# Kernel optimization log

Measured on AMD Instinct MI355X. Metric: run time of the kernel, lower is better.

Reference implementation:

```python
import jax, jax.numpy as jnp
import numpy as np

N, D, H2, E = 4096, 1024, 4096, 8  # tokens, input_dim, 2*hidden_dim, num_experts
H = H2 // 2


def setup_inputs() -> dict:
    key = jax.random.key(0)
    k1, k2, k3 = jax.random.split(key, 3)
    x = jax.random.normal(k1, (N, D), dtype=jnp.float32)
    expert_weights = jax.random.normal(k2, (E, D, H2), dtype=jnp.float32) * (1.0 / np.sqrt(D))
    expert_indices = jax.random.randint(k3, (N,), 0, E, dtype=jnp.int32)
    return {"x": x, "expert_weights": expert_weights, "expert_indices": expert_indices}


def reference(x, expert_weights, expert_indices):
    # Grouped GEMM equivalent: each token n is processed by expert e = expert_indices[n]:
    #   h_n = x_n @ W_e            -> [2H]
    #   out_n = silu(h[:H]) * h[H:] (SwiGLU)
    # jit-friendly dense-dispatch: project with all experts, then gather the assigned one.
    h_all = jnp.einsum('nd,edh->neh', x, expert_weights)            # [N, E, 2H]
    h = jnp.take_along_axis(h_all, expert_indices[:, None, None].astype(jnp.int32), axis=1)[:, 0]  # [N, 2H]
    a, b = h[:, :H], h[:, H:]
    return jax.nn.silu(a) * b                                        # [N, H]
```

## Files before the change

kernel.cpp:

```cpp
#include <hip/hip_runtime.h>
#include <hip/hip_bf16.h>

#define N_TOK 4096
#define DIM   1024
#define H2V   4096
#define HV    2048
#define NE    8
#define BM    128
#define BN    64
#define BK    64
#define NTHR  256
#define KSTEPS (DIM / BK)
#define ROW_TILES (N_TOK / BM)

#define WS_COUNTS 0
#define WS_BASE   64
#define WS_SLOTS  128
#define WS_XPERM  66560

typedef __attribute__((ext_vector_type(4))) float  f32x4;
typedef __attribute__((ext_vector_type(8))) short  s16x8;

__device__ __forceinline__ unsigned short f2bf(float f) {
    union { __hip_bfloat16 h; unsigned short u; } v;
    v.h = __float2bfloat16(f);
    return v.u;
}

__global__ void k_init(int* __restrict__ counts) {
    if (threadIdx.x < NE) counts[threadIdx.x] = 0;
}

__global__ void k_scatter(const int* __restrict__ idx, int* __restrict__ counts,
                          unsigned short* __restrict__ slots) {
    int n = blockIdx.x * blockDim.x + threadIdx.x;
    if (n < N_TOK) {
        int e = idx[n];
        int p = atomicAdd(&counts[e], 1);
        slots[e * N_TOK + p] = (unsigned short)n;
    }
}

__global__ void k_base(const int* __restrict__ counts, int* __restrict__ base) {
    if (threadIdx.x == 0) {
        int b = 0;
#pragma unroll
        for (int e = 0; e < NE; ++e) { base[e] = b; b += counts[e]; }
        base[NE] = b;
    }
}

__global__ void k_gather(const float* __restrict__ X, const int* __restrict__ base,
                         const unsigned short* __restrict__ slots,
                         unsigned short* __restrict__ Xp) {
    const int r    = blockIdx.x * 4 + (threadIdx.x >> 6);
    const int lane = threadIdx.x & 63;
    int e = 0;
#pragma unroll
    for (int i = 0; i < NE - 1; ++i) if (r >= base[i + 1]) e = i + 1;
    const int tok = slots[e * N_TOK + (r - base[e])];
    const float* src = X + (size_t)tok * DIM + lane * 16;
    unsigned short* dst = Xp + (size_t)r * DIM + lane * 16;
    f32x4 v0 = *(const f32x4*)(src);
    f32x4 v1 = *(const f32x4*)(src + 4);
    f32x4 v2 = *(const f32x4*)(src + 8);
    f32x4 v3 = *(const f32x4*)(src + 12);
    unsigned short t0[8], t1[8];
#pragma unroll
    for (int i = 0; i < 4; ++i) { t0[i] = f2bf(v0[i]); t0[4 + i] = f2bf(v1[i]); }
#pragma unroll
    for (int i = 0; i < 4; ++i) { t1[i] = f2bf(v2[i]); t1[4 + i] = f2bf(v3[i]); }
    *(s16x8*)(dst)     = *(const s16x8*)t0;
    *(s16x8*)(dst + 8) = *(const s16x8*)t1;
}

__global__ __launch_bounds__(NTHR, 3) void k_gemm(
        const float* __restrict__ W, const int* __restrict__ counts,
        const int* __restrict__ base, const unsigned short* __restrict__ slots,
        const unsigned short* __restrict__ Xp, float* __restrict__ out) {
    const int ct = blockIdx.x;
    const int e  = blockIdx.y >> 5;
    const int rt = blockIdx.y & 31;
    const int cnt = counts[e];
    const int tbase = rt * BM;
    if (tbase >= cnt) return;
    const int row_g0 = base[e] + tbase;

    __shared__ unsigned short As[2][BM * BK];
    __shared__ unsigned short Bs[2 * BN * BK];

    const int t    = threadIdx.x;
    const int lane = t & 63;
    const int wid  = t >> 6;
    const int wm   = wid >> 1;
    const int wn   = wid & 1;
    const int l16  = lane & 15;
    const int g16  = lane >> 4;

    const unsigned short* aptr[4];
#pragma unroll
    for (int j = 0; j < 4; ++j) {
        int i  = wid * 4 + j;
        int rl = i * 8 + (lane >> 3);
        int qs = (lane & 7) ^ ((lane >> 3) & 7);
        aptr[j] = Xp + (size_t)(row_g0 + rl) * DIM + qs * 8;
    }
    const int c0 = (t & 31) * 4;
    const int ko = t >> 5;
    const int gc = ct * BN + (c0 & 63) + (c0 >> 6) * HV;
    const float* bptr = W + (size_t)e * DIM * H2V + (size_t)(ko * 8) * H2V + gc;

    f32x4 acc[2][4][2];
    const f32x4 zero = {0.f, 0.f, 0.f, 0.f};
#pragma unroll
    for (int g = 0; g < 2; ++g)
#pragma unroll
        for (int m = 0; m < 4; ++m)
#pragma unroll
            for (int n = 0; n < 2; ++n) acc[g][m][n] = zero;

    f32x4 bv[8];

    auto issueA = [&](int ks, int buf) {
#pragma unroll
        for (int j = 0; j < 4; ++j) {
            const unsigned short* g = aptr[j] + ks * BK;
            unsigned short* l = (unsigned short*)&As[buf][(wid * 4 + j) * 512];
            __builtin_amdgcn_global_load_lds(
                (const __attribute__((address_space(1))) unsigned int*)(const void*)g,
                (__attribute__((address_space(3))) unsigned int*)(void*)l, 16, 0, 0);
        }
    };
    auto loadB = [&](int ks) {
#pragma unroll
        for (int i = 0; i < 8; ++i)
            bv[i] = *(const f32x4*)(bptr + (size_t)(ks * BK + i) * H2V);
    };
    auto storeB = [&]() {
#pragma unroll
        for (int j = 0; j < 4; ++j) {
            int c = c0 + j;
            int key = ((c >> 1) ^ (c >> 4)) & 7;
            unsigned short tmp[8];
#pragma unroll
            for (int i = 0; i < 8; ++i) tmp[i] = f2bf(bv[i][j]);
            *(s16x8*)&Bs[c * 64 + ((ko ^ key) * 8)] = *(const s16x8*)tmp;
        }
    };

    issueA(0, 0);
    loadB(0);

    for (int ks = 0; ks < KSTEPS; ++ks) {
        const int cur = ks & 1;
        asm volatile("s_waitcnt vmcnt(0)" ::: "memory");
        __builtin_amdgcn_s_barrier();
        storeB();
        if (ks + 1 < KSTEPS) {
            issueA(ks + 1, cur ^ 1);
            loadB(ks + 1);
        }
        asm volatile("s_waitcnt lgkmcnt(0)" ::: "memory");
        __builtin_amdgcn_s_barrier();
#pragma unroll
        for (int kk = 0; kk < 2; ++kk) {
            const int gran = kk * 4 + g16;
            s16x8 af[4], bfr[2][2];
#pragma unroll
            for (int m = 0; m < 4; ++m) {
                int row = wm * 64 + m * 16 + l16;
                af[m] = *(const s16x8*)&As[cur][row * 64 + ((gran ^ (row & 7)) * 8)];
            }
#pragma unroll
            for (int g = 0; g < 2; ++g)
#pragma unroll
                for (int n = 0; n < 2; ++n) {
                    int c = g * BN + wn * 32 + n * 16 + l16;
                    int key = ((c >> 1) ^ (c >> 4)) & 7;
                    bfr[g][n] = *(const s16x8*)&Bs[c * 64 + ((gran ^ key) * 8)];
                }
#pragma unroll
            for (int g = 0; g < 2; ++g)
#pragma unroll
                for (int m = 0; m < 4; ++m)
#pragma unroll
                    for (int n = 0; n < 2; ++n)
                        acc[g][m][n] = __builtin_amdgcn_mfma_f32_16x16x32_bf16(
                            af[m], bfr[g][n], acc[g][m][n], 0, 0, 0);
        }
    }

    const unsigned short* ids = slots + e * N_TOK;
#pragma unroll
    for (int m = 0; m < 4; ++m) {
#pragma unroll
        for (int r = 0; r < 4; ++r) {
            int rowt = wm * 64 + m * 16 + g16 * 4 + r;
            int slot = tbase + rowt;
            if (slot < cnt) {
                int tok = ids[slot];
#pragma unroll
                for (int n = 0; n < 2; ++n) {
                    int col = ct * BN + wn * 32 + n * 16 + l16;
                    float a = acc[0][m][n][r];
                    float b = acc[1][m][n][r];
                    float sg = a / (1.0f + __expf(-a));
                    out[(size_t)tok * HV + col] = sg * b;
                }
            }
        }
    }
}

extern "C" void kernel_launch(void* const* d_in, const int* in_sizes, int n_in,
                              void* d_out, int out_size, void* d_ws, size_t ws_size,
                              hipStream_t stream) {
    const float* X  = (const float*)d_in[0];
    const float* W  = (const float*)d_in[1];
    const int* idx  = (const int*)d_in[2];
    float* out      = (float*)d_out;

    int* counts = (int*)((char*)d_ws + WS_COUNTS);
    int* base   = (int*)((char*)d_ws + WS_BASE);
    unsigned short* slots = (unsigned short*)((char*)d_ws + WS_SLOTS);
    unsigned short* Xp    = (unsigned short*)((char*)d_ws + WS_XPERM);

    k_init<<<1, 64, 0, stream>>>(counts);
    k_scatter<<<N_TOK / 256, 256, 0, stream>>>(idx, counts, slots);
    k_base<<<1, 64, 0, stream>>>(counts, base);
    k_gather<<<N_TOK / 4, 256, 0, stream>>>(X, base, slots, Xp);
    dim3 grid(HV / BN, NE * ROW_TILES);
    k_gemm<<<grid, NTHR, 0, stream>>>(W, counts, base, slots, Xp, out);
}
```

Before: 96.59 us.

## Double-buffer B tile in LDS and prefetch weights two K-steps ahead

Adds a second LDS buffer for the converted weight tile and restructures the main loop into a software pipeline. The weight load now runs two K-steps ahead, with partial vmcnt waits, and the A and B stores overlap the MFMA phase. The MFMA block runs at raised wave priority, and launch bounds drop from 3 to 2 waves per SIMD to make room for the extra registers and LDS. The goal is to hide global-load and fp32-to-bf16 conversion latency behind matrix math, at the cost of lower occupancy and 64KB of LDS per block.

```diff
diff --git a/kernel.cpp b/kernel.cpp
--- a/kernel.cpp
+++ b/kernel.cpp
@@ -74,7 +74,7 @@
     *(s16x8*)(dst + 8) = *(const s16x8*)t1;
 }
 
-__global__ __launch_bounds__(NTHR, 3) void k_gemm(
+__global__ __launch_bounds__(NTHR, 2) void k_gemm(
         const float* __restrict__ W, const int* __restrict__ counts,
         const int* __restrict__ base, const unsigned short* __restrict__ slots,
         const unsigned short* __restrict__ Xp, float* __restrict__ out) {
@@ -87,7 +87,7 @@
     const int row_g0 = base[e] + tbase;
 
     __shared__ unsigned short As[2][BM * BK];
-    __shared__ unsigned short Bs[2 * BN * BK];
+    __shared__ unsigned short Bs[2][2 * BN * BK];
 
     const int t    = threadIdx.x;
     const int lane = t & 63;
@@ -136,7 +136,7 @@
         for (int i = 0; i < 8; ++i)
             bv[i] = *(const f32x4*)(bptr + (size_t)(ks * BK + i) * H2V);
     };
-    auto storeB = [&]() {
+    auto storeB = [&](int buf) {
 #pragma unroll
         for (int j = 0; j < 4; ++j) {
             int c = c0 + j;
@@ -144,24 +144,11 @@
             unsigned short tmp[8];
 #pragma unroll
             for (int i = 0; i < 8; ++i) tmp[i] = f2bf(bv[i][j]);
-            *(s16x8*)&Bs[c * 64 + ((ko ^ key) * 8)] = *(const s16x8*)tmp;
-        }
-    };
-
-    issueA(0, 0);
-    loadB(0);
-
-    for (int ks = 0; ks < KSTEPS; ++ks) {
-        const int cur = ks & 1;
-        asm volatile("s_waitcnt vmcnt(0)" ::: "memory");
-        __builtin_amdgcn_s_barrier();
-        storeB();
-        if (ks + 1 < KSTEPS) {
-            issueA(ks + 1, cur ^ 1);
-            loadB(ks + 1);
-        }
-        asm volatile("s_waitcnt lgkmcnt(0)" ::: "memory");
-        __builtin_amdgcn_s_barrier();
+            *(s16x8*)&Bs[buf][c * 64 + ((ko ^ key) * 8)] = *(const s16x8*)tmp;
+        }
+    };
+    auto mfmaPhase = [&](int cur) {
+        __builtin_amdgcn_s_setprio(1);
 #pragma unroll
         for (int kk = 0; kk < 2; ++kk) {
             const int gran = kk * 4 + g16;
@@ -177,7 +164,7 @@
                 for (int n = 0; n < 2; ++n) {
                     int c = g * BN + wn * 32 + n * 16 + l16;
                     int key = ((c >> 1) ^ (c >> 4)) & 7;
-                    bfr[g][n] = *(const s16x8*)&Bs[c * 64 + ((gran ^ key) * 8)];
+                    bfr[g][n] = *(const s16x8*)&Bs[cur][c * 64 + ((gran ^ key) * 8)];
                 }
 #pragma unroll
             for (int g = 0; g < 2; ++g)
@@ -187,6 +174,38 @@
                     for (int n = 0; n < 2; ++n)
                         acc[g][m][n] = __builtin_amdgcn_mfma_f32_16x16x32_bf16(
                             af[m], bfr[g][n], acc[g][m][n], 0, 0, 0);
+        }
+        __builtin_amdgcn_s_setprio(0);
+    };
+
+    loadB(0);
+    issueA(0, 0);
+    asm volatile("s_waitcnt vmcnt(0)" ::: "memory");
+    __builtin_amdgcn_sched_barrier(0);
+    storeB(0);
+    loadB(1);
+    asm volatile("s_waitcnt lgkmcnt(0)" ::: "memory");
+    __builtin_amdgcn_sched_barrier(0);
+
+#pragma unroll 2
+    for (int ks = 0; ks < KSTEPS; ++ks) {
+        const int cur = ks & 1;
+        if (ks == KSTEPS - 1) {
+            asm volatile("s_waitcnt vmcnt(0)" ::: "memory");
+        } else {
+            asm volatile("s_waitcnt vmcnt(8)" ::: "memory");
+        }
+        __builtin_amdgcn_sched_barrier(0);
+        __builtin_amdgcn_s_barrier();
+        if (ks + 1 < KSTEPS) issueA(ks + 1, cur ^ 1);
+        mfmaPhase(cur);
+        if (ks + 1 < KSTEPS) {
+            asm volatile("s_waitcnt vmcnt(4)" ::: "memory");
+            __builtin_amdgcn_sched_barrier(0);
+            storeB(cur ^ 1);
+            if (ks + 2 < KSTEPS) loadB(ks + 2);
+            asm volatile("s_waitcnt lgkmcnt(0)" ::: "memory");
+            __builtin_amdgcn_sched_barrier(0);
         }
     }
 
```

Result: slower. 106.2 us (+10.0%).
